# Performance work log

Measured on AMD Instinct MI355X. Metric: run time of the kernel, lower is better.

The kernel has to match this reference:

```python
import jax, jax.numpy as jnp
import numpy as np

N = 50000        # nodes
DEG = 32         # in-degree per node
E = N * DEG      # edges
T = 4            # towers
NODE = 128       # node_dim
OUT = 128        # out_dim
IN_T = NODE // T   # 32, divide_input tower slice
OUT_T = OUT // T   # 32
AVG_D_LOG = float(np.log(5.0))  # avg_d = {'log': log(4+1)}
EPS = 1e-5


def setup_inputs() -> dict:
    key = jax.random.key(0)
    ks = jax.random.split(key, 6)
    h = jax.random.normal(ks[0], (N, NODE), jnp.float32)
    src = jax.random.randint(ks[1], (E,), 0, N)
    # every node gets exactly DEG incoming edges (sorted dst)
    dst = jnp.repeat(jnp.arange(N), DEG)
    # per-tower pretrans MLP (1 layer): Linear(2*IN_T -> OUT_T)
    W_pre = jax.random.normal(ks[2], (T, 2 * IN_T, OUT_T), jnp.float32) * 0.05
    b_pre = jnp.zeros((T, OUT_T), jnp.float32)
    # per-tower posttrans MLP (1 layer): Linear(12*OUT_T + IN_T -> OUT_T)
    W_post = jax.random.normal(ks[3], (T, 12 * OUT_T + IN_T, OUT_T), jnp.float32) * 0.05
    b_post = jnp.zeros((T, OUT_T), jnp.float32)
    # mixing network: Linear(OUT -> OUT) + LeakyReLU
    W_mix = jax.random.normal(ks[4], (OUT, OUT), jnp.float32) * 0.05
    b_mix = jnp.zeros((OUT,), jnp.float32)
    return dict(h=h, src=src, dst=dst, W_pre=W_pre, b_pre=b_pre,
                W_post=W_post, b_post=b_post, W_mix=W_mix, b_mix=b_mix)


def _pna_forward(h, src, dst, W_pre, b_pre, W_post, b_post, W_mix, b_mix):
    ht = h.reshape(N, T, IN_T)                    # divide_input: tower slices
    z2 = jnp.concatenate([ht[src], ht[dst]], axis=-1)   # [E,T,2*IN_T] (src||dst)
    # pretrans: MLP(1 layer) then ReLU
    e = jax.nn.relu(jnp.einsum('etk,tko->eto', z2, W_pre) + b_pre)  # [E,T,OUT_T]

    deg = jax.ops.segment_sum(jnp.ones((E,), h.dtype), dst, num_segments=N)  # [N]
    deg_c = jnp.maximum(deg, 1.0)[:, None, None]
    seg = lambda x: jax.ops.segment_sum(x, dst, num_segments=N)
    mean = seg(e) / deg_c                          # [N,T,OUT_T]
    mean_sq = seg(e * e) / deg_c
    std = jnp.sqrt(jax.nn.relu(mean_sq - mean * mean) + EPS)
    mx = jax.ops.segment_max(e, dst, num_segments=N)
    mn = jax.ops.segment_min(e, dst, num_segments=N)
    agg = jnp.concatenate([mean, mx, mn, std], axis=-1)   # [N,T,4*OUT_T]

    # scalers: identity, amplification, attenuation (D = in-degree)
    sc = jnp.log(deg + 1.0) / AVG_D_LOG            # [N]
    amp = agg * sc[:, None, None]
    att = agg / jnp.maximum(sc, EPS)[:, None, None]
    h_agg = jnp.concatenate([agg, amp, att], axis=-1)     # [N,T,12*OUT_T]

    # posttrans: cat(h_tower, aggregated) -> MLP(1 layer) -> ReLU
    z = jnp.concatenate([ht, h_agg], axis=-1)      # [N,T,IN_T+12*OUT_T]
    hp = jax.nn.relu(jnp.einsum('ntk,tko->nto', z, W_post) + b_post)  # [N,T,OUT_T]
    h_cat = hp.reshape(N, OUT)

    h_out = jax.nn.leaky_relu(h_cat @ W_mix + b_mix, 0.01)
    return h + h_out                               # residual (node_dim == out_dim)


def reference(h, src, dst, W_pre, b_pre, W_post, b_post, W_mix, b_mix):
    return _pna_forward(h, src, dst, W_pre, b_pre, W_post, b_post, W_mix, b_mix)
```

## Files before the change

### kernel.cpp

```cpp
#include <hip/hip_runtime.h>
#include <hip/hip_bf16.h>
#include <math.h>

#define N_NODES 50000
#define DEG     32
#define NBP     25
#define EPSV    1e-5f

typedef __attribute__((ext_vector_type(8))) short short8;
typedef __attribute__((ext_vector_type(4))) float f32x4;

__global__ void k_prep(const float* __restrict__ W_post, const float* __restrict__ W_mix,
                       __hip_bfloat16* __restrict__ WeffT, __hip_bfloat16* __restrict__ WmixT,
                       float sc, float isc) {
    int i = blockIdx.x * 256 + threadIdx.x;
    if (i < 4 * 32 * 160) {
        int k = i % 160, to = i / 160, o = to & 31, t = to >> 5;
        const float* Wt = W_post + t * 416 * 32;
        float v;
        if (k < 32) v = Wt[k * 32 + o];
        else {
            int g = k - 32;
            v = Wt[(32 + g) * 32 + o] + sc * Wt[(160 + g) * 32 + o] + isc * Wt[(288 + g) * 32 + o];
        }
        WeffT[i] = __float2bfloat16(v);
    }
    int j = i - 4 * 32 * 160;
    if (j >= 0 && j < 128 * 128) {
        int k = j & 127, o = j >> 7;
        WmixT[j] = __float2bfloat16(W_mix[k * 128 + o]);
    }
}

__global__ __launch_bounds__(128) void k_proj(const float* __restrict__ h,
        const float* __restrict__ W_pre, const float* __restrict__ b_pre,
        __hip_bfloat16* __restrict__ Pd, __hip_bfloat16* __restrict__ Ps) {
    int c = threadIdx.x, t = c >> 5, o = c & 31;
    const float* Wt = W_pre + t * 64 * 32;
    float wsr[32], wdr[32];
#pragma unroll
    for (int k = 0; k < 32; ++k) { wsr[k] = Wt[k * 32 + o]; wdr[k] = Wt[(32 + k) * 32 + o]; }
    float bp = b_pre[t * 32 + o];
    __shared__ float sh[128];
    int base = blockIdx.x * NBP;
    for (int ni = 0; ni < NBP; ++ni) {
        int n = base + ni;
        __syncthreads();
        sh[c] = h[n * 128 + c];
        __syncthreads();
        const float4* h4 = (const float4*)(sh + t * 32);
        float as = 0.f, ad = 0.f;
#pragma unroll
        for (int k4 = 0; k4 < 8; ++k4) {
            float4 hv = h4[k4];
            as = fmaf(hv.x, wsr[4*k4+0], as); ad = fmaf(hv.x, wdr[4*k4+0], ad);
            as = fmaf(hv.y, wsr[4*k4+1], as); ad = fmaf(hv.y, wdr[4*k4+1], ad);
            as = fmaf(hv.z, wsr[4*k4+2], as); ad = fmaf(hv.z, wdr[4*k4+2], ad);
            as = fmaf(hv.w, wsr[4*k4+3], as); ad = fmaf(hv.w, wdr[4*k4+3], ad);
        }
        Ps[n * 128 + c] = __float2bfloat16(as);
        Pd[n * 128 + c] = __float2bfloat16(ad + bp);
    }
}

__global__ __launch_bounds__(256) void k_fused(const float* __restrict__ h,
        const int* __restrict__ src, const __hip_bfloat16* __restrict__ Pd,
        const __hip_bfloat16* __restrict__ Ps, const __hip_bfloat16* __restrict__ WeffT,
        const __hip_bfloat16* __restrict__ WmixT, const float* __restrict__ b_post,
        const float* __restrict__ b_mix, float* __restrict__ out) {
    __shared__ __align__(16) __hip_bfloat16 sZ[32][648];
    __shared__ __align__(16) __hip_bfloat16 sHp[32][136];
    int tid = threadIdx.x, w = tid >> 6, lane = tid & 63;
    int nb = blockIdx.x * 32;

    int c0 = 2 * lane;
    int tA = c0 >> 5, oA = c0 & 31;
#pragma unroll
    for (int r = 0; r < 8; ++r) {
        int row = r * 4 + w;
        int n = nb + row;
        __hip_bfloat16* zr = &sZ[row][tA * 160 + oA];
        if (n < N_NODES) {
            int vsrc = src[n * DEG + (lane & 31)];
            float2 hv = *(const float2*)(h + n * 128 + c0);
            unsigned int pdu = *(const unsigned int*)(Pd + n * 128 + c0);
            float pd0 = __uint_as_float(pdu << 16);
            float pd1 = __uint_as_float(pdu & 0xffff0000u);
            float sum0 = 0.f, sum1 = 0.f, sq0 = 0.f, sq1 = 0.f;
            float mx0 = -1e30f, mx1 = -1e30f, mn0 = 1e30f, mn1 = 1e30f;
#pragma unroll
            for (int j0 = 0; j0 < DEG; j0 += 8) {
                unsigned int pv[8];
#pragma unroll
                for (int u = 0; u < 8; ++u) {
                    int s = __builtin_amdgcn_readlane(vsrc, j0 + u);
                    pv[u] = *(const unsigned int*)(Ps + s * 128 + c0);
                }
#pragma unroll
                for (int u = 0; u < 8; ++u) {
                    float f0 = __uint_as_float(pv[u] << 16);
                    float f1 = __uint_as_float(pv[u] & 0xffff0000u);
                    float e0 = fmaxf(f0 + pd0, 0.f);
                    float e1 = fmaxf(f1 + pd1, 0.f);
                    sum0 += e0; sq0 = fmaf(e0, e0, sq0);
                    mx0 = fmaxf(mx0, e0); mn0 = fminf(mn0, e0);
                    sum1 += e1; sq1 = fmaf(e1, e1, sq1);
                    mx1 = fmaxf(mx1, e1); mn1 = fminf(mn1, e1);
                }
            }
            float mean0 = sum0 * (1.f / DEG), mean1 = sum1 * (1.f / DEG);
            float sd0 = sqrtf(fmaxf(sq0 * (1.f / DEG) - mean0 * mean0, 0.f) + EPSV);
            float sd1 = sqrtf(fmaxf(sq1 * (1.f / DEG) - mean1 * mean1, 0.f) + EPSV);
            zr[0]   = __float2bfloat16(hv.x);  zr[1]   = __float2bfloat16(hv.y);
            zr[32]  = __float2bfloat16(mean0); zr[33]  = __float2bfloat16(mean1);
            zr[64]  = __float2bfloat16(mx0);   zr[65]  = __float2bfloat16(mx1);
            zr[96]  = __float2bfloat16(mn0);   zr[97]  = __float2bfloat16(mn1);
            zr[128] = __float2bfloat16(sd0);   zr[129] = __float2bfloat16(sd1);
        } else {
            *(unsigned int*)(zr)       = 0u; *(unsigned int*)(zr + 32) = 0u;
            *(unsigned int*)(zr + 64)  = 0u; *(unsigned int*)(zr + 96) = 0u;
            *(unsigned int*)(zr + 128) = 0u;
        }
    }
    __syncthreads();

    int col = lane & 15, quad = lane >> 4;
    int r0 = (w & 1) * 16;
    int ctb = (w >> 1) * 4;
#pragma unroll
    for (int i = 0; i < 4; ++i) {
        int ct = ctb + i, t = ct >> 1, nt = ct & 1;
        f32x4 acc = {0.f, 0.f, 0.f, 0.f};
        int oc = t * 32 + nt * 16 + col;
        const __hip_bfloat16* wrow = WeffT + oc * 160 + quad * 8;
#pragma unroll
        for (int ks = 0; ks < 5; ++ks) {
            short8 a = *(const short8*)(&sZ[r0 + col][t * 160 + ks * 32 + quad * 8]);
            short8 b = *(const short8*)(wrow + ks * 32);
            acc = __builtin_amdgcn_mfma_f32_16x16x32_bf16(a, b, acc, 0, 0, 0);
        }
        float bp = b_post[oc];
#pragma unroll
        for (int r = 0; r < 4; ++r)
            sHp[r0 + quad * 4 + r][oc] = __float2bfloat16(fmaxf(acc[r] + bp, 0.f));
    }
    __syncthreads();

#pragma unroll
    for (int i = 0; i < 4; ++i) {
        int nt = ctb + i;
        f32x4 acc = {0.f, 0.f, 0.f, 0.f};
        int oc = nt * 16 + col;
        const __hip_bfloat16* wrow = WmixT + oc * 128 + quad * 8;
#pragma unroll
        for (int ks = 0; ks < 4; ++ks) {
            short8 a = *(const short8*)(&sHp[r0 + col][ks * 32 + quad * 8]);
            short8 b = *(const short8*)(wrow + ks * 32);
            acc = __builtin_amdgcn_mfma_f32_16x16x32_bf16(a, b, acc, 0, 0, 0);
        }
        float bm = b_mix[oc];
#pragma unroll
        for (int r = 0; r < 4; ++r) {
            int n = nb + r0 + quad * 4 + r;
            if (n < N_NODES) {
                float m = acc[r] + bm;
                m = m > 0.f ? m : 0.01f * m;
                out[n * 128 + oc] = h[n * 128 + oc] + m;
            }
        }
    }
}

extern "C" void kernel_launch(void* const* d_in, const int* in_sizes, int n_in,
                              void* d_out, int out_size, void* d_ws, size_t ws_size,
                              hipStream_t stream) {
    const float* h      = (const float*)d_in[0];
    const int*   src    = (const int*)d_in[1];
    const float* W_pre  = (const float*)d_in[3];
    const float* b_pre  = (const float*)d_in[4];
    const float* W_post = (const float*)d_in[5];
    const float* b_post = (const float*)d_in[6];
    const float* W_mix  = (const float*)d_in[7];
    const float* b_mix  = (const float*)d_in[8];
    float* out = (float*)d_out;

    char* ws = (char*)d_ws;
    __hip_bfloat16* WeffT = (__hip_bfloat16*)ws;
    __hip_bfloat16* WmixT = (__hip_bfloat16*)(ws + 40960);
    __hip_bfloat16* Pd    = (__hip_bfloat16*)(ws + 73728);
    __hip_bfloat16* Ps    = (__hip_bfloat16*)(ws + 73728 + 12800000);

    double scd = log(33.0) / log(5.0);
    float sc = (float)scd, isc = (float)(1.0 / scd);

    hipLaunchKernelGGL(k_prep, dim3(144), dim3(256), 0, stream, W_post, W_mix, WeffT, WmixT, sc, isc);
    hipLaunchKernelGGL(k_proj, dim3(N_NODES / NBP), dim3(128), 0, stream, h, W_pre, b_pre, Pd, Ps);
    hipLaunchKernelGGL(k_fused, dim3((N_NODES + 31) / 32), dim3(256), 0, stream,
                       h, src, Pd, Ps, WeffT, WmixT, b_post, b_mix, out);
}
```

Baseline: 198.9 us.

## Split projection threads by src/dst half and shrink fused block tile to 16 nodes

k_proj now runs 256 threads, with each half computing only the src or the dst projection. It stages 8 nodes of h per barrier using float4 loads, which halves the weight registers per thread and cuts barrier count. k_fused processes 16 nodes per block instead of 32, which doubles the grid, and removes the tail-bound checks because 50000 divides evenly by 16. It also packs the bf16 pairs into 32-bit LDS stores. This raises block count and occupancy for the gather-bound stage, at the cost of fewer MFMA tiles per block and more redundant weight loads.

```diff
diff --git a/kernel.cpp b/kernel.cpp
--- a/kernel.cpp
+++ b/kernel.cpp
@@ -4,7 +4,8 @@
 
 #define N_NODES 50000
 #define DEG     32
-#define NBP     25
+#define NBP     40
+#define NBF     16
 #define EPSV    1e-5f
 
 typedef __attribute__((ext_vector_type(8))) short short8;
@@ -32,34 +33,45 @@
     }
 }
 
-__global__ __launch_bounds__(128) void k_proj(const float* __restrict__ h,
+__global__ __launch_bounds__(256) void k_proj(const float* __restrict__ h,
         const float* __restrict__ W_pre, const float* __restrict__ b_pre,
         __hip_bfloat16* __restrict__ Pd, __hip_bfloat16* __restrict__ Ps) {
-    int c = threadIdx.x, t = c >> 5, o = c & 31;
-    const float* Wt = W_pre + t * 64 * 32;
-    float wsr[32], wdr[32];
-#pragma unroll
-    for (int k = 0; k < 32; ++k) { wsr[k] = Wt[k * 32 + o]; wdr[k] = Wt[(32 + k) * 32 + o]; }
-    float bp = b_pre[t * 32 + o];
-    __shared__ float sh[128];
+    int tid = threadIdx.x;
+    int c = tid & 127, half = tid >> 7;
+    int t = c >> 5, o = c & 31;
+    const float* Wt = W_pre + t * 64 * 32 + half * 32 * 32;
+    float wr[32];
+#pragma unroll
+    for (int k = 0; k < 32; ++k) wr[k] = Wt[k * 32 + o];
+    float bp = half ? b_pre[t * 32 + o] : 0.f;
+    __shared__ float sh[8][128];
     int base = blockIdx.x * NBP;
-    for (int ni = 0; ni < NBP; ++ni) {
-        int n = base + ni;
+    for (int r = 0; r < NBP / 8; ++r) {
+        int n0 = base + r * 8;
         __syncthreads();
-        sh[c] = h[n * 128 + c];
+        ((float4*)sh)[tid] = ((const float4*)(h + n0 * 128))[tid];
         __syncthreads();
-        const float4* h4 = (const float4*)(sh + t * 32);
-        float as = 0.f, ad = 0.f;
-#pragma unroll
-        for (int k4 = 0; k4 < 8; ++k4) {
-            float4 hv = h4[k4];
-            as = fmaf(hv.x, wsr[4*k4+0], as); ad = fmaf(hv.x, wdr[4*k4+0], ad);
-            as = fmaf(hv.y, wsr[4*k4+1], as); ad = fmaf(hv.y, wdr[4*k4+1], ad);
-            as = fmaf(hv.z, wsr[4*k4+2], as); ad = fmaf(hv.z, wdr[4*k4+2], ad);
-            as = fmaf(hv.w, wsr[4*k4+3], as); ad = fmaf(hv.w, wdr[4*k4+3], ad);
-        }
-        Ps[n * 128 + c] = __float2bfloat16(as);
-        Pd[n * 128 + c] = __float2bfloat16(ad + bp);
+        float acc[8];
+#pragma unroll
+        for (int ni = 0; ni < 8; ++ni) {
+            const float4* h4 = (const float4*)(&sh[ni][t * 32]);
+            float a = 0.f;
+#pragma unroll
+            for (int k4 = 0; k4 < 8; ++k4) {
+                float4 hv = h4[k4];
+                a = fmaf(hv.x, wr[4*k4+0], a);
+                a = fmaf(hv.y, wr[4*k4+1], a);
+                a = fmaf(hv.z, wr[4*k4+2], a);
+                a = fmaf(hv.w, wr[4*k4+3], a);
+            }
+            acc[ni] = a;
+        }
+#pragma unroll
+        for (int ni = 0; ni < 8; ++ni) {
+            int n = n0 + ni;
+            if (half) Pd[n * 128 + c] = __float2bfloat16(acc[ni] + bp);
+            else      Ps[n * 128 + c] = __float2bfloat16(acc[ni]);
+        }
     }
 }
 
@@ -68,105 +80,99 @@
         const __hip_bfloat16* __restrict__ Ps, const __hip_bfloat16* __restrict__ WeffT,
         const __hip_bfloat16* __restrict__ WmixT, const float* __restrict__ b_post,
         const float* __restrict__ b_mix, float* __restrict__ out) {
-    __shared__ __align__(16) __hip_bfloat16 sZ[32][648];
-    __shared__ __align__(16) __hip_bfloat16 sHp[32][136];
+    __shared__ __align__(16) __hip_bfloat16 sZ[NBF][648];
+    __shared__ __align__(16) __hip_bfloat16 sHp[NBF][136];
     int tid = threadIdx.x, w = tid >> 6, lane = tid & 63;
-    int nb = blockIdx.x * 32;
+    int nb = blockIdx.x * NBF;
 
     int c0 = 2 * lane;
     int tA = c0 >> 5, oA = c0 & 31;
 #pragma unroll
-    for (int r = 0; r < 8; ++r) {
+    for (int r = 0; r < 4; ++r) {
         int row = r * 4 + w;
         int n = nb + row;
-        __hip_bfloat16* zr = &sZ[row][tA * 160 + oA];
-        if (n < N_NODES) {
-            int vsrc = src[n * DEG + (lane & 31)];
-            float2 hv = *(const float2*)(h + n * 128 + c0);
-            unsigned int pdu = *(const unsigned int*)(Pd + n * 128 + c0);
-            float pd0 = __uint_as_float(pdu << 16);
-            float pd1 = __uint_as_float(pdu & 0xffff0000u);
-            float sum0 = 0.f, sum1 = 0.f, sq0 = 0.f, sq1 = 0.f;
-            float mx0 = -1e30f, mx1 = -1e30f, mn0 = 1e30f, mn1 = 1e30f;
-#pragma unroll
-            for (int j0 = 0; j0 < DEG; j0 += 8) {
-                unsigned int pv[8];
-#pragma unroll
-                for (int u = 0; u < 8; ++u) {
-                    int s = __builtin_amdgcn_readlane(vsrc, j0 + u);
-                    pv[u] = *(const unsigned int*)(Ps + s * 128 + c0);
-                }
-#pragma unroll
-                for (int u = 0; u < 8; ++u) {
-                    float f0 = __uint_as_float(pv[u] << 16);
-                    float f1 = __uint_as_float(pv[u] & 0xffff0000u);
-                    float e0 = fmaxf(f0 + pd0, 0.f);
-                    float e1 = fmaxf(f1 + pd1, 0.f);
-                    sum0 += e0; sq0 = fmaf(e0, e0, sq0);
-                    mx0 = fmaxf(mx0, e0); mn0 = fminf(mn0, e0);
-                    sum1 += e1; sq1 = fmaf(e1, e1, sq1);
-                    mx1 = fmaxf(mx1, e1); mn1 = fminf(mn1, e1);
-                }
+        int vsrc = src[n * DEG + (lane & 31)];
+        float2 hv = *(const float2*)(h + n * 128 + c0);
+        unsigned int pdu = *(const unsigned int*)(Pd + n * 128 + c0);
+        float pd0 = __uint_as_float(pdu << 16);
+        float pd1 = __uint_as_float(pdu & 0xffff0000u);
+        float sum0 = 0.f, sum1 = 0.f, sq0 = 0.f, sq1 = 0.f;
+        float mx0 = -1e30f, mx1 = -1e30f, mn0 = 1e30f, mn1 = 1e30f;
+#pragma unroll
+        for (int j0 = 0; j0 < DEG; j0 += 8) {
+            unsigned int pv[8];
+#pragma unroll
+            for (int u = 0; u < 8; ++u) {
+                int s = __builtin_amdgcn_readlane(vsrc, j0 + u);
+                pv[u] = *(const unsigned int*)(Ps + s * 128 + c0);
             }
-            float mean0 = sum0 * (1.f / DEG), mean1 = sum1 * (1.f / DEG);
-            float sd0 = sqrtf(fmaxf(sq0 * (1.f / DEG) - mean0 * mean0, 0.f) + EPSV);
-            float sd1 = sqrtf(fmaxf(sq1 * (1.f / DEG) - mean1 * mean1, 0.f) + EPSV);
-            zr[0]   = __float2bfloat16(hv.x);  zr[1]   = __float2bfloat16(hv.y);
-            zr[32]  = __float2bfloat16(mean0); zr[33]  = __float2bfloat16(mean1);
-            zr[64]  = __float2bfloat16(mx0);   zr[65]  = __float2bfloat16(mx1);
-            zr[96]  = __float2bfloat16(mn0);   zr[97]  = __float2bfloat16(mn1);
-            zr[128] = __float2bfloat16(sd0);   zr[129] = __float2bfloat16(sd1);
-        } else {
-            *(unsigned int*)(zr)       = 0u; *(unsigned int*)(zr + 32) = 0u;
-            *(unsigned int*)(zr + 64)  = 0u; *(unsigned int*)(zr + 96) = 0u;
-            *(unsigned int*)(zr + 128) = 0u;
-        }
+#pragma unroll
+            for (int u = 0; u < 8; ++u) {
+                float f0 = __uint_as_float(pv[u] << 16);
+                float f1 = __uint_as_float(pv[u] & 0xffff0000u);
+                float e0 = fmaxf(f0 + pd0, 0.f);
+                float e1 = fmaxf(f1 + pd1, 0.f);
+                sum0 += e0; sq0 = fmaf(e0, e0, sq0);
+                mx0 = fmaxf(mx0, e0); mn0 = fminf(mn0, e0);
+                sum1 += e1; sq1 = fmaf(e1, e1, sq1);
+                mx1 = fmaxf(mx1, e1); mn1 = fminf(mn1, e1);
+            }
+        }
+        float mean0 = sum0 * (1.f / DEG), mean1 = sum1 * (1.f / DEG);
+        float sd0 = sqrtf(fmaxf(sq0 * (1.f / DEG) - mean0 * mean0, 0.f) + EPSV);
+        float sd1 = sqrtf(fmaxf(sq1 * (1.f / DEG) - mean1 * mean1, 0.f) + EPSV);
+        unsigned int* zr = (unsigned int*)(&sZ[row][tA * 160 + oA]);
+        auto pack = [](float a, float b) {
+            return (unsigned int)(__bfloat16_as_ushort(__float2bfloat16(a))) |
+                   ((unsigned int)(__bfloat16_as_ushort(__float2bfloat16(b))) << 16);
+        };
+        zr[0]  = pack(hv.x, hv.y);
+        zr[16] = pack(mean0, mean1);
+        zr[32] = pack(mx0, mx1);
+        zr[48] = pack(mn0, mn1);
+        zr[64] = pack(sd0, sd1);
     }
     __syncthreads();
 
     int col = lane & 15, quad = lane >> 4;
-    int r0 = (w & 1) * 16;
-    int ctb = (w >> 1) * 4;
-#pragma unroll
-    for (int i = 0; i < 4; ++i) {
-        int ct = ctb + i, t = ct >> 1, nt = ct & 1;
+#pragma unroll
+    for (int i = 0; i < 2; ++i) {
+        int ct = w * 2 + i, t = ct >> 1, nt = ct & 1;
         f32x4 acc = {0.f, 0.f, 0.f, 0.f};
         int oc = t * 32 + nt * 16 + col;
         const __hip_bfloat16* wrow = WeffT + oc * 160 + quad * 8;
 #pragma unroll
         for (int ks = 0; ks < 5; ++ks) {
-            short8 a = *(const short8*)(&sZ[r0 + col][t * 160 + ks * 32 + quad * 8]);
+            short8 a = *(const short8*)(&sZ[col][t * 160 + ks * 32 + quad * 8]);
             short8 b = *(const short8*)(wrow + ks * 32);
             acc = __builtin_amdgcn_mfma_f32_16x16x32_bf16(a, b, acc, 0, 0, 0);
         }
         float bp = b_post[oc];
 #pragma unroll
         for (int r = 0; r < 4; ++r)
-            sHp[r0 + quad * 4 + r][oc] = __float2bfloat16(fmaxf(acc[r] + bp, 0.f));
+            sHp[quad * 4 + r][oc] = __float2bfloat16(fmaxf(acc[r] + bp, 0.f));
     }
     __syncthreads();
 
 #pragma unroll
-    for (int i = 0; i < 4; ++i) {
-        int nt = ctb + i;
+    for (int i = 0; i < 2; ++i) {
+        int nt = w * 2 + i;
         f32x4 acc = {0.f, 0.f, 0.f, 0.f};
         int oc = nt * 16 + col;
         const __hip_bfloat16* wrow = WmixT + oc * 128 + quad * 8;
 #pragma unroll
         for (int ks = 0; ks < 4; ++ks) {
-            short8 a = *(const short8*)(&sHp[r0 + col][ks * 32 + quad * 8]);
+            short8 a = *(const short8*)(&sHp[col][ks * 32 + quad * 8]);
             short8 b = *(const short8*)(wrow + ks * 32);
             acc = __builtin_amdgcn_mfma_f32_16x16x32_bf16(a, b, acc, 0, 0, 0);
         }
         float bm = b_mix[oc];
 #pragma unroll
         for (int r = 0; r < 4; ++r) {
-            int n = nb + r0 + quad * 4 + r;
-            if (n < N_NODES) {
-                float m = acc[r] + bm;
-                m = m > 0.f ? m : 0.01f * m;
-                out[n * 128 + oc] = h[n * 128 + oc] + m;
-            }
+            int n = nb + quad * 4 + r;
+            float m = acc[r] + bm;
+            m = m > 0.f ? m : 0.01f * m;
+            out[n * 128 + oc] = h[n * 128 + oc] + m;
         }
     }
 }
@@ -194,7 +200,7 @@
     float sc = (float)scd, isc = (float)(1.0 / scd);
 
     hipLaunchKernelGGL(k_prep, dim3(144), dim3(256), 0, stream, W_post, W_mix, WeffT, WmixT, sc, isc);
-    hipLaunchKernelGGL(k_proj, dim3(N_NODES / NBP), dim3(128), 0, stream, h, W_pre, b_pre, Pd, Ps);
-    hipLaunchKernelGGL(k_fused, dim3((N_NODES + 31) / 32), dim3(256), 0, stream,
+    hipLaunchKernelGGL(k_proj, dim3(N_NODES / NBP), dim3(256), 0, stream, h, W_pre, b_pre, Pd, Ps);
+    hipLaunchKernelGGL(k_fused, dim3(N_NODES / NBF), dim3(256), 0, stream,
                        h, src, Pd, Ps, WeffT, WmixT, b_post, b_mix, out);
 }
```

New measurement: 178.6 us. 10.2% less time.
